# Kernel optimization log

Measured on AMD Instinct MI355X. Metric: run time of the kernel, lower is better.

## Reference

```python
import jax, jax.numpy as jnp
import numpy as np

OUT, IN = 11008, 4096
GROUP = 128
NUM_GROUPS = IN // GROUP  # 32
PACKED = OUT * IN // 2
TOKENS = 4096


def setup_inputs() -> dict:
    key = jax.random.key(0)
    k1, k2, k3, k4 = jax.random.split(key, 4)
    x = jax.random.normal(k1, (TOKENS, IN), dtype=jnp.float32)
    # packed bytes: two int4 values per byte (low nibble = even index)
    w_packed = jax.random.randint(k2, (PACKED,), 0, 256, dtype=jnp.int32)
    # per-(out_channel, group) scale and integer zero-point
    w_scale = jax.random.uniform(k3, (OUT, NUM_GROUPS), dtype=jnp.float32) * 0.02 + 1e-3
    w_zero = jax.random.randint(k4, (OUT, NUM_GROUPS), 0, 16, dtype=jnp.int32)
    return {"x": x, "w_packed": w_packed, "w_scale": w_scale, "w_zero": w_zero}


def _dequant_weight(w_packed, w_scale, w_zero):
    out_features, num_groups = w_scale.shape
    in_features = (w_packed.shape[0] * 2) // out_features
    group = in_features // num_groups
    # unpack nibbles: element 2i -> low nibble, element 2i+1 -> high nibble
    low = w_packed & 15
    high = (w_packed >> 4) & 15
    w4 = jnp.stack([low, high], axis=-1).reshape(out_features, in_features)
    # signed int4: values >= 8 map to value - 16
    w4 = jnp.where(w4 >= 8, w4 - 16, w4).astype(jnp.float32)
    # per-group dequant: (w - zero) * scale
    wg = w4.reshape(out_features, num_groups, group)
    w = (wg - w_zero.astype(jnp.float32)[:, :, None]) * w_scale[:, :, None]
    return w.reshape(out_features, in_features)


def reference(x, w_packed, w_scale, w_zero):
    w = _dequant_weight(w_packed, w_scale, w_zero)  # [OUT, IN]
    return x @ w.T  # [TOKENS, OUT]
```

## Files before the change

### kernel.cpp

```cpp
#include <hip/hip_runtime.h>
#include <stdint.h>
#include <stddef.h>


#define M_TOK 4096
#define K_IN  4096
#define N_OUT 11008
#define QGROUPS 32
#define MT 32
#define NT 86
#define TILES (MT * NT)
#define PER_XCD (TILES / 8)

#define BT_OFF   ((size_t)M_TOK * K_IN * 2)
#define CTR_OFF  (BT_OFF + 23068672)

typedef _Float16 h8v __attribute__((ext_vector_type(8)));
typedef float    f4v __attribute__((ext_vector_type(4)));

__device__ __forceinline__ void gload16(const void* g, void* l) {
  __builtin_amdgcn_global_load_lds(
      (__attribute__((address_space(1))) void*)(g),
      (__attribute__((address_space(3))) void*)(l),
      16, 0, 0);
}

__global__ __launch_bounds__(256) void cvt_x_kernel(const float* __restrict__ x,
                                                    _Float16* __restrict__ xh) {
  size_t t = (size_t)blockIdx.x * 256 + threadIdx.x;
  const float4* s = (const float4*)x + t * 2;
  float4 a = s[0], b = s[1];
  h8v o;
  o[0] = (_Float16)a.x; o[1] = (_Float16)a.z; o[2] = (_Float16)b.x; o[3] = (_Float16)b.z;
  o[4] = (_Float16)a.y; o[5] = (_Float16)a.w; o[6] = (_Float16)b.y; o[7] = (_Float16)b.w;
  ((h8v*)xh)[t] = o;
}

__global__ __launch_bounds__(256) void repack_w_kernel(const int* __restrict__ wp,
                                                       uint32_t* __restrict__ bt) {
  size_t tg = (size_t)blockIdx.x * 256 + threadIdx.x;
  int tid = (int)(tg & 255);
  int kt  = (int)((tg >> 8) & 63);
  int t   = (int)(tg >> 14);
  int row = t * 128 + (tid >> 1);
  const int4* src = (const int4*)(wp + (size_t)row * 2048 + kt * 32 + (tid & 1) * 16);
  uint32_t d[4];
#pragma unroll
  for (int j = 0; j < 4; ++j) {
    int4 v = src[j];
    d[j] = (((uint32_t)v.x & 255u) | (((uint32_t)v.y & 255u) << 8) |
            (((uint32_t)v.z & 255u) << 16) | (((uint32_t)v.w & 255u) << 24)) ^ 0x88888888u;
  }
  uint4 o; o.x = d[0]; o.y = d[1]; o.z = d[2]; o.w = d[3];
  ((uint4*)bt)[tg] = o;
}

__global__ __launch_bounds__(256, 2) void gemm_kernel(
    const _Float16* __restrict__ Ah,
    const uint32_t* __restrict__ Bt,
    const float* __restrict__ WS,
    const int* __restrict__ WZ,
    unsigned int* __restrict__ ctr,
    float* __restrict__ C) {
  __shared__ __align__(16) short As[128 * 64];
  __shared__ __align__(16) short Bs[128 * 64];
  __shared__ int tileId;

  const int tid = threadIdx.x;
  if (tid == 0) {
    int xcd = __builtin_amdgcn_s_getreg(63508) & 7;
    int got = -1;
#pragma unroll 1
    for (int off = 0; off < 8; ++off) {
      int x = (xcd + off) & 7;
      unsigned idx = atomicAdd(&ctr[x], 1u);
      if (idx < PER_XCD) { got = x * PER_XCD + (int)idx; break; }
    }
    tileId = got;
  }
  __syncthreads();
  const int tl = tileId;
  const int x  = tl / PER_XCD;
  const int e  = tl - x * PER_XCD;
  const int r  = e / NT;
  const int nt = e - r * NT;
  const int m0 = (x + 8 * r) * 128;
  const int n0 = nt * 128;

  const int lane = tid & 63;
  const int wid  = tid >> 6;
  const int wm = (wid >> 1) * 64;
  const int wn = (wid & 1) * 64;
  const int quad = lane >> 4;
  const int lrow = lane & 15;
  const int sw = lrow & 7;
  const int srl = lane >> 3;
  const int skb = (lane & 7) ^ srl;
  const int brow = tid >> 1;
  const int bhalf = tid & 1;

  f4v acc[4][4];
#pragma unroll
  for (int i = 0; i < 4; ++i)
#pragma unroll
    for (int j = 0; j < 4; ++j) acc[i][j] = (f4v){0.f, 0.f, 0.f, 0.f};

  const uint4* bsrc = (const uint4*)Bt + (size_t)nt * 64 * 256 + tid;
  const int sbase = (n0 + brow) * QGROUPS;

  uint4 pw = bsrc[0];
  for (int kt = 0; kt < 64; ++kt) {
    int ktn = (kt < 63) ? kt + 1 : 63;
    uint4 pn = bsrc[(size_t)ktn * 256];
    int g = kt >> 1;
    float s  = WS[sbase + g];
    float zf = (float)WZ[sbase + g];

    __syncthreads();
#pragma unroll
    for (int j = 0; j < 4; ++j) {
      int slab = wid * 4 + j;
      int row = slab * 8 + srl;
      gload16(Ah + (size_t)(m0 + row) * K_IN + kt * 64 + skb * 8,
              (char*)As + slab * 1024);
    }
    {
      _Float16 sh = (_Float16)s;
      _Float16 ch = (_Float16)(-s * (136.0f + zf));
      h8v sv8, cv8;
#pragma unroll
      for (int i = 0; i < 8; ++i) { sv8[i] = sh; cv8[i] = ch; }
      uint32_t wv[4] = {pw.x, pw.y, pw.z, pw.w};
#pragma unroll
      for (int j = 0; j < 4; ++j) {
        uint32_t w = wv[j];
        uint32_t ea = (w & 0x0F0F0F0Fu) << 3;
        uint32_t eb = (w >> 1) & 0x78787878u;
        union { uint32_t d[4]; h8v v; } u;
        u.d[0] = __builtin_amdgcn_perm(0x58585858u, ea, 0x04010400u);
        u.d[1] = __builtin_amdgcn_perm(0x58585858u, ea, 0x04030402u);
        u.d[2] = __builtin_amdgcn_perm(0x58585858u, eb, 0x04010400u);
        u.d[3] = __builtin_amdgcn_perm(0x58585858u, eb, 0x04030402u);
        u.v = __builtin_elementwise_fma(u.v, sv8, cv8);
        int kb = bhalf * 4 + j;
        int unit = brow * 8 + (kb ^ (brow & 7));
        *(h8v*)((char*)Bs + unit * 16) = u.v;
      }
    }
    __syncthreads();

#pragma unroll
    for (int ks = 0; ks < 2; ++ks) {
      h8v af[4], bf[4];
#pragma unroll
      for (int mi = 0; mi < 4; ++mi) {
        int unit = (wm + mi * 16 + lrow) * 8 + ((ks * 4 + quad) ^ sw);
        af[mi] = *(const h8v*)((char*)As + unit * 16);
      }
#pragma unroll
      for (int ni = 0; ni < 4; ++ni) {
        int unit = (wn + ni * 16 + lrow) * 8 + ((ks * 4 + quad) ^ sw);
        bf[ni] = *(const h8v*)((char*)Bs + unit * 16);
      }
#pragma unroll
      for (int mi = 0; mi < 4; ++mi)
#pragma unroll
        for (int ni = 0; ni < 4; ++ni)
          acc[mi][ni] = __builtin_amdgcn_mfma_f32_16x16x32_f16(
              af[mi], bf[ni], acc[mi][ni], 0, 0, 0);
    }
    pw = pn;
  }

#pragma unroll
  for (int mi = 0; mi < 4; ++mi) {
#pragma unroll
    for (int rr = 0; rr < 4; ++rr) {
      int m = m0 + wm + mi * 16 + quad * 4 + rr;
      float* crow = C + (size_t)m * N_OUT + n0 + wn + lrow;
#pragma unroll
      for (int ni = 0; ni < 4; ++ni) crow[ni * 16] = acc[mi][ni][rr];
    }
  }
}

extern "C" void kernel_launch(void* const* d_in, const int* in_sizes, int n_in,
                              void* d_out, int out_size, void* d_ws, size_t ws_size,
                              hipStream_t stream) {
  const float* x   = (const float*)d_in[0];
  const int*   wp  = (const int*)d_in[1];
  const float* wsc = (const float*)d_in[2];
  const int*   wz  = (const int*)d_in[3];
  float* out = (float*)d_out;

  _Float16* Ah = (_Float16*)d_ws;
  uint32_t* Bt = (uint32_t*)((char*)d_ws + BT_OFF);
  unsigned int* ctr = (unsigned int*)((char*)d_ws + CTR_OFF);

  hipMemsetAsync(ctr, 0, 8 * sizeof(unsigned int), stream);
  cvt_x_kernel<<<(M_TOK * (size_t)K_IN) / (8 * 256), 256, 0, stream>>>(x, Ah);
  repack_w_kernel<<<(size_t)NT * 64, 256, 0, stream>>>(wp, Bt);
  gemm_kernel<<<TILES, 256, 0, stream>>>(Ah, Bt, wsc, wz, ctr, out);
}
```

Measured before the change: 715.3 us.

## Pre-dequantize weights to fp16 and use 256x256 double-buffered GEMM tiles

Replaces the in-loop int4 dequant with a separate kernel that writes a full fp16 weight matrix. The GEMM then becomes a plain fp16 GEMM with 256x256 tiles, 512 threads, and a double-buffered LDS pipeline. That pipeline uses direct global-to-LDS loads, fine-grained phases with partial vmcnt waits, and s_setprio around the MFMA blocks. Atomic XCD tile scheduling is dropped in favour of a static swizzle. The trade-off is extra memory traffic for the fp16 weights (about 90 MB written and then read) and 128 KB of LDS per block, which constrains occupancy.

```diff
diff --git a/kernel.cpp b/kernel.cpp
--- a/kernel.cpp
+++ b/kernel.cpp
@@ -6,14 +6,13 @@
 #define M_TOK 4096
 #define K_IN  4096
 #define N_OUT 11008
-#define QGROUPS 32
-#define MT 32
-#define NT 86
-#define TILES (MT * NT)
-#define PER_XCD (TILES / 8)
+#define NGRP  32
 
-#define BT_OFF   ((size_t)M_TOK * K_IN * 2)
-#define CTR_OFF  (BT_OFF + 23068672)
+#define MTI 16
+#define NTI 43
+#define TILES (MTI * NTI)
+
+#define BH_OFF ((size_t)M_TOK * K_IN * 2)
 
 typedef _Float16 h8v __attribute__((ext_vector_type(8)));
 typedef float    f4v __attribute__((ext_vector_type(4)));
@@ -25,163 +24,162 @@
       16, 0, 0);
 }
 
+#define MEMFENCE asm volatile("" ::: "memory")
+__device__ __forceinline__ void bar() {
+  MEMFENCE;
+  __builtin_amdgcn_s_barrier();
+  MEMFENCE;
+}
+#define WAIT_VM4 asm volatile("s_waitcnt vmcnt(4)" ::: "memory")
+
 __global__ __launch_bounds__(256) void cvt_x_kernel(const float* __restrict__ x,
                                                     _Float16* __restrict__ xh) {
   size_t t = (size_t)blockIdx.x * 256 + threadIdx.x;
   const float4* s = (const float4*)x + t * 2;
   float4 a = s[0], b = s[1];
   h8v o;
-  o[0] = (_Float16)a.x; o[1] = (_Float16)a.z; o[2] = (_Float16)b.x; o[3] = (_Float16)b.z;
-  o[4] = (_Float16)a.y; o[5] = (_Float16)a.w; o[6] = (_Float16)b.y; o[7] = (_Float16)b.w;
+  o[0] = (_Float16)a.x; o[1] = (_Float16)a.y; o[2] = (_Float16)a.z; o[3] = (_Float16)a.w;
+  o[4] = (_Float16)b.x; o[5] = (_Float16)b.y; o[6] = (_Float16)b.z; o[7] = (_Float16)b.w;
   ((h8v*)xh)[t] = o;
 }
 
-__global__ __launch_bounds__(256) void repack_w_kernel(const int* __restrict__ wp,
-                                                       uint32_t* __restrict__ bt) {
+__global__ __launch_bounds__(256) void dequant_w_kernel(const int* __restrict__ wp,
+                                                        const float* __restrict__ ws,
+                                                        const int* __restrict__ wz,
+                                                        _Float16* __restrict__ bh) {
   size_t tg = (size_t)blockIdx.x * 256 + threadIdx.x;
-  int tid = (int)(tg & 255);
-  int kt  = (int)((tg >> 8) & 63);
-  int t   = (int)(tg >> 14);
-  int row = t * 128 + (tid >> 1);
-  const int4* src = (const int4*)(wp + (size_t)row * 2048 + kt * 32 + (tid & 1) * 16);
-  uint32_t d[4];
+  int j   = (int)(tg & 127);
+  int row = (int)(tg >> 7);
+  int g = j >> 2;
+  float s = ws[(size_t)row * NGRP + g];
+  float c = -s * (8.0f + (float)wz[(size_t)row * NGRP + g]);
+  const int4* src = (const int4*)(wp + (size_t)row * 2048 + j * 16);
+  _Float16* dst = bh + (size_t)row * 4096 + j * 32;
 #pragma unroll
-  for (int j = 0; j < 4; ++j) {
-    int4 v = src[j];
-    d[j] = (((uint32_t)v.x & 255u) | (((uint32_t)v.y & 255u) << 8) |
-            (((uint32_t)v.z & 255u) << 16) | (((uint32_t)v.w & 255u) << 24)) ^ 0x88888888u;
+  for (int b = 0; b < 4; ++b) {
+    int4 v = src[b];
+    int q[4] = {v.x, v.y, v.z, v.w};
+    h8v o;
+#pragma unroll
+    for (int i = 0; i < 4; ++i) {
+      int lo = (q[i] & 15) ^ 8;
+      int hi = ((q[i] >> 4) & 15) ^ 8;
+      o[2 * i]     = (_Float16)(s * (float)lo + c);
+      o[2 * i + 1] = (_Float16)(s * (float)hi + c);
+    }
+    ((h8v*)dst)[b] = o;
   }
-  uint4 o; o.x = d[0]; o.y = d[1]; o.z = d[2]; o.w = d[3];
-  ((uint4*)bt)[tg] = o;
 }
 
-__global__ __launch_bounds__(256, 2) void gemm_kernel(
+__global__ __launch_bounds__(512, 2) void gemm_kernel(
     const _Float16* __restrict__ Ah,
-    const uint32_t* __restrict__ Bt,
-    const float* __restrict__ WS,
-    const int* __restrict__ WZ,
-    unsigned int* __restrict__ ctr,
+    const _Float16* __restrict__ Bh,
     float* __restrict__ C) {
-  __shared__ __align__(16) short As[128 * 64];
-  __shared__ __align__(16) short Bs[128 * 64];
-  __shared__ int tileId;
+  __shared__ __align__(128) char smem[131072];
 
-  const int tid = threadIdx.x;
-  if (tid == 0) {
-    int xcd = __builtin_amdgcn_s_getreg(63508) & 7;
-    int got = -1;
-#pragma unroll 1
-    for (int off = 0; off < 8; ++off) {
-      int x = (xcd + off) & 7;
-      unsigned idx = atomicAdd(&ctr[x], 1u);
-      if (idx < PER_XCD) { got = x * PER_XCD + (int)idx; break; }
-    }
-    tileId = got;
-  }
-  __syncthreads();
-  const int tl = tileId;
-  const int x  = tl / PER_XCD;
-  const int e  = tl - x * PER_XCD;
-  const int r  = e / NT;
-  const int nt = e - r * NT;
-  const int m0 = (x + 8 * r) * 128;
-  const int n0 = nt * 128;
+  const int bid = blockIdx.x;
+  const int swz = (bid & 7) * 86 + (bid >> 3);
+  const int mt = swz / NTI;
+  const int nt = swz - mt * NTI;
+  const int m0 = mt * 256;
+  const int n0 = nt * 256;
 
+  const int tid  = threadIdx.x;
   const int lane = tid & 63;
   const int wid  = tid >> 6;
-  const int wm = (wid >> 1) * 64;
-  const int wn = (wid & 1) * 64;
+  const int wm   = wid >> 2;
+  const int wn   = wid & 3;
+  const int lrow = lane & 15;
   const int quad = lane >> 4;
-  const int lrow = lane & 15;
-  const int sw = lrow & 7;
-  const int srl = lane >> 3;
-  const int skb = (lane & 7) ^ srl;
-  const int brow = tid >> 1;
-  const int bhalf = tid & 1;
 
-  f4v acc[4][4];
+  const int r0  = wid * 32 + (lane >> 2);
+  const int kc2 = (lane & 3) ^ ((lane >> 2) & 3);
+  const size_t gA0 = (size_t)(m0 + r0) * K_IN + kc2 * 8;
+  const size_t gB0 = (size_t)(n0 + r0) * K_IN + kc2 * 8;
+  const int ldsl = wid * 2048;
+
+  const int su   = quad ^ (lrow & 3);
+  const int aoff = ((wm * 128 + lrow) * 4 + su) * 16;
+  const int boff = 32768 + ((wn * 64 + lrow) * 4 + su) * 16;
+
+  f4v acc[8][4];
 #pragma unroll
-  for (int i = 0; i < 4; ++i)
+  for (int i = 0; i < 8; ++i)
 #pragma unroll
     for (int j = 0; j < 4; ++j) acc[i][j] = (f4v){0.f, 0.f, 0.f, 0.f};
 
-  const uint4* bsrc = (const uint4*)Bt + (size_t)nt * 64 * 256 + tid;
-  const int sbase = (n0 + brow) * QGROUPS;
+#define STAGE_A(NXT, KT, KH)                                                   \
+  { const _Float16* g_ = Ah + gA0 + (size_t)(KT) * 64 + (KH) * 32;             \
+    char* l_ = smem + (NXT) * 65536 + (KH) * 16384 + ldsl;                     \
+    gload16(g_, l_);                                                           \
+    gload16(g_ + 16 * K_IN, l_ + 1024); }
 
-  uint4 pw = bsrc[0];
-  for (int kt = 0; kt < 64; ++kt) {
-    int ktn = (kt < 63) ? kt + 1 : 63;
-    uint4 pn = bsrc[(size_t)ktn * 256];
-    int g = kt >> 1;
-    float s  = WS[sbase + g];
-    float zf = (float)WZ[sbase + g];
+#define STAGE_B(NXT, KT, KH)                                                   \
+  { const _Float16* g_ = Bh + gB0 + (size_t)(KT) * 64 + (KH) * 32;             \
+    char* l_ = smem + (NXT) * 65536 + 32768 + (KH) * 16384 + ldsl;             \
+    gload16(g_, l_);                                                           \
+    gload16(g_ + 16 * K_IN, l_ + 1024); }
 
-    __syncthreads();
-#pragma unroll
-    for (int j = 0; j < 4; ++j) {
-      int slab = wid * 4 + j;
-      int row = slab * 8 + srl;
-      gload16(Ah + (size_t)(m0 + row) * K_IN + kt * 64 + skb * 8,
-              (char*)As + slab * 1024);
-    }
-    {
-      _Float16 sh = (_Float16)s;
-      _Float16 ch = (_Float16)(-s * (136.0f + zf));
-      h8v sv8, cv8;
-#pragma unroll
-      for (int i = 0; i < 8; ++i) { sv8[i] = sh; cv8[i] = ch; }
-      uint32_t wv[4] = {pw.x, pw.y, pw.z, pw.w};
-#pragma unroll
-      for (int j = 0; j < 4; ++j) {
-        uint32_t w = wv[j];
-        uint32_t ea = (w & 0x0F0F0F0Fu) << 3;
-        uint32_t eb = (w >> 1) & 0x78787878u;
-        union { uint32_t d[4]; h8v v; } u;
-        u.d[0] = __builtin_amdgcn_perm(0x58585858u, ea, 0x04010400u);
-        u.d[1] = __builtin_amdgcn_perm(0x58585858u, ea, 0x04030402u);
-        u.d[2] = __builtin_amdgcn_perm(0x58585858u, eb, 0x04010400u);
-        u.d[3] = __builtin_amdgcn_perm(0x58585858u, eb, 0x04030402u);
-        u.v = __builtin_elementwise_fma(u.v, sv8, cv8);
-        int kb = bhalf * 4 + j;
-        int unit = brow * 8 + (kb ^ (brow & 7));
-        *(h8v*)((char*)Bs + unit * 16) = u.v;
-      }
-    }
-    __syncthreads();
+  h8v af[4], bf[4];
 
-#pragma unroll
-    for (int ks = 0; ks < 2; ++ks) {
-      h8v af[4], bf[4];
-#pragma unroll
-      for (int mi = 0; mi < 4; ++mi) {
-        int unit = (wm + mi * 16 + lrow) * 8 + ((ks * 4 + quad) ^ sw);
-        af[mi] = *(const h8v*)((char*)As + unit * 16);
-      }
-#pragma unroll
-      for (int ni = 0; ni < 4; ++ni) {
-        int unit = (wn + ni * 16 + lrow) * 8 + ((ks * 4 + quad) ^ sw);
-        bf[ni] = *(const h8v*)((char*)Bs + unit * 16);
-      }
-#pragma unroll
-      for (int mi = 0; mi < 4; ++mi)
-#pragma unroll
-        for (int ni = 0; ni < 4; ++ni)
-          acc[mi][ni] = __builtin_amdgcn_mfma_f32_16x16x32_f16(
-              af[mi], bf[ni], acc[mi][ni], 0, 0, 0);
-    }
-    pw = pn;
+#define PHASE(CUR, KS, MH, DO_STAGE, DO_VM)                                    \
+  {                                                                            \
+    const char* sec_ = smem + (CUR) * 65536 + (KS) * 16384;                    \
+    if ((MH) == 0) {                                                           \
+      _Pragma("unroll")                                                        \
+      for (int nf = 0; nf < 4; ++nf)                                           \
+        bf[nf] = *(const h8v*)(sec_ + boff + nf * 1024);                       \
+    }                                                                          \
+    _Pragma("unroll")                                                          \
+    for (int i = 0; i < 4; ++i)                                                \
+      af[i] = *(const h8v*)(sec_ + aoff + (MH) * 4096 + i * 1024);             \
+    DO_STAGE;                                                                  \
+    if (DO_VM) { WAIT_VM4; }                                                   \
+    bar();                                                                     \
+    __builtin_amdgcn_s_setprio(1);                                             \
+    _Pragma("unroll")                                                          \
+    for (int mi = 0; mi < 4; ++mi)                                             \
+      _Pragma("unroll")                                                        \
+      for (int nf = 0; nf < 4; ++nf)                                           \
+        acc[(MH) * 4 + mi][nf] = __builtin_amdgcn_mfma_f32_16x16x32_f16(       \
+            af[mi], bf[nf], acc[(MH) * 4 + mi][nf], 0, 0, 0);                  \
+    __builtin_amdgcn_s_setprio(0);                                             \
+    bar();                                                                     \
+  }
+
+  STAGE_A(0, 0, 0);
+  STAGE_B(0, 0, 0);
+  STAGE_A(0, 0, 1);
+  STAGE_B(0, 0, 1);
+  WAIT_VM4;
+  bar();
+
+  for (int t = 0; t < 64; t += 2) {
+    const int t1 = t + 1;
+    const int t2 = (t + 2 < 64) ? t + 2 : 63;
+    PHASE(0, 0, 0, STAGE_A(1, t1, 0), 0)
+    PHASE(0, 0, 1, STAGE_B(1, t1, 0), 1)
+    PHASE(0, 1, 0, STAGE_A(1, t1, 1), 0)
+    PHASE(0, 1, 1, STAGE_B(1, t1, 1), 1)
+    PHASE(1, 0, 0, STAGE_A(0, t2, 0), 0)
+    PHASE(1, 0, 1, STAGE_B(0, t2, 0), 1)
+    PHASE(1, 1, 0, STAGE_A(0, t2, 1), 0)
+    PHASE(1, 1, 1, STAGE_B(0, t2, 1), 1)
   }
 
 #pragma unroll
-  for (int mi = 0; mi < 4; ++mi) {
+  for (int mf = 0; mf < 8; ++mf) {
 #pragma unroll
     for (int rr = 0; rr < 4; ++rr) {
-      int m = m0 + wm + mi * 16 + quad * 4 + rr;
-      float* crow = C + (size_t)m * N_OUT + n0 + wn + lrow;
+      int m = m0 + wm * 128 + mf * 16 + quad * 4 + rr;
+      float* crow = C + (size_t)m * N_OUT + n0 + wn * 64 + lrow;
 #pragma unroll
-      for (int ni = 0; ni < 4; ++ni) crow[ni * 16] = acc[mi][ni][rr];
+      for (int nf = 0; nf < 4; ++nf) crow[nf * 16] = acc[mf][nf][rr];
     }
   }
+#undef PHASE
+#undef STAGE_A
+#undef STAGE_B
 }
 
 extern "C" void kernel_launch(void* const* d_in, const int* in_sizes, int n_in,
@@ -191,14 +189,11 @@
   const int*   wp  = (const int*)d_in[1];
   const float* wsc = (const float*)d_in[2];
   const int*   wz  = (const int*)d_in[3];
-  float* out = (float*)d_out;
 
   _Float16* Ah = (_Float16*)d_ws;
-  uint32_t* Bt = (uint32_t*)((char*)d_ws + BT_OFF);
-  unsigned int* ctr = (unsigned int*)((char*)d_ws + CTR_OFF);
+  _Float16* Bh = (_Float16*)((char*)d_ws + BH_OFF);
 
-  hipMemsetAsync(ctr, 0, 8 * sizeof(unsigned int), stream);
   cvt_x_kernel<<<(M_TOK * (size_t)K_IN) / (8 * 256), 256, 0, stream>>>(x, Ah);
-  repack_w_kernel<<<(size_t)NT * 64, 256, 0, stream>>>(wp, Bt);
-  gemm_kernel<<<TILES, 256, 0, stream>>>(Ah, Bt, wsc, wz, ctr, out);
+  dequant_w_kernel<<<((size_t)N_OUT * 128) / 256, 256, 0, stream>>>(wp, wsc, wz, Bh);
+  gemm_kernel<<<TILES, 512, 0, stream>>>(Ah, Bh, (float*)d_out);
 }
```

Result: faster. 651.1 us (-9.0%).
